# Kernel optimization log

Measured on AMD Instinct MI355X. Metric: run time of the kernel, lower is better.

The kernel has to match this reference:

```python
import jax, jax.numpy as jnp
import numpy as np

B, C, IMG, P = 64, 3, 224, 16
S = P // 2
G = IMG // P                      # 14 patches per side
NP = G * G                        # 196
N = NP + 1                        # +cls token
DIM, DEPTH, H, DH = 384, 12, 12, 32
INNER = H * DH                    # 384
MLP, NCLS = 1536, 1000
PD = 7 * P * P                    # patch_dim = 1792
EPS = 1e-5


def layernorm(x, g, b):
    mu = x.mean(-1, keepdims=True)
    var = ((x - mu) ** 2).mean(-1, keepdims=True)
    return (x - mu) * jax.lax.rsqrt(var + EPS) * g + b


def setup_inputs() -> dict:
    key = jax.random.key(0)
    ks = jax.random.split(key, 24)
    nrm = lambda k, shp, sc: jax.random.normal(k, shp, jnp.float32) * sc
    d = {
        "img": nrm(ks[0], (B, C, IMG, IMG), 1.0),
        "patch_w": nrm(ks[1], (DIM, PD), 0.02),
        "patch_b": jnp.zeros((DIM,), jnp.float32),
        "pos_emb": nrm(ks[2], (1, N, DIM), 0.02),
        "cls_tok": nrm(ks[3], (1, 1, DIM), 0.02),
        "ln1_g": jnp.ones((DEPTH, DIM), jnp.float32),
        "ln1_b": jnp.zeros((DEPTH, DIM), jnp.float32),
        "qkv_w": nrm(ks[4], (DEPTH, 3 * INNER, DIM), 0.02),
        "scale": jax.random.uniform(ks[5], (DEPTH, H), jnp.float32),
        "out_w": nrm(ks[6], (DEPTH, DIM, INNER), 0.02),
        "out_b": jnp.zeros((DEPTH, DIM), jnp.float32),
        "ln2_g": jnp.ones((DEPTH, DIM), jnp.float32),
        "ln2_b": jnp.zeros((DEPTH, DIM), jnp.float32),
        "ff_w1": nrm(ks[7], (DEPTH, MLP, DIM), 0.02),
        "ff_b1": jnp.zeros((DEPTH, MLP), jnp.float32),
        "ff_w2": nrm(ks[8], (DEPTH, DIM, MLP), 0.02),
        "ff_b2": jnp.zeros((DEPTH, DIM), jnp.float32),
        "lnf_g": jnp.ones((DIM,), jnp.float32),
        "lnf_b": jnp.zeros((DIM,), jnp.float32),
        "head_w": nrm(ks[9], (NCLS, DIM), 0.02),
        "head_b": jnp.zeros((NCLS,), jnp.float32),
    }
    return d


def reference(img, patch_w, patch_b, pos_emb, cls_tok, ln1_g, ln1_b, qkv_w,
              scale, out_w, out_b, ln2_g, ln2_b, ff_w1, ff_b1, ff_w2, ff_b2,
              lnf_g, lnf_b, head_w, head_b):
    # --- PatchShifting: pad, channel-mean, 4 shifted crops, concat to 7ch ---
    xp = jnp.pad(img, ((0, 0), (0, 0), (S, S), (S, S)))
    m = xp.mean(axis=1, keepdims=True)                     # [B,1,H+2S,W+2S]
    x_l2 = m[:, :, S:-S, : -2 * S]
    x_r2 = m[:, :, S:-S, 2 * S:]
    x_t2 = m[:, :, : -2 * S, S:-S]
    x_b2 = m[:, :, 2 * S:, S:-S]
    xc = jnp.concatenate([img, x_l2, x_r2, x_t2, x_b2], axis=1)  # [B,7,IMG,IMG]
    # --- patchify: b c (h p1) (w p2) -> b (h w) (p1 p2 c) ---
    patches = xc.reshape(B, 7, G, P, G, P).transpose(0, 2, 4, 3, 5, 1).reshape(B, NP, PD)
    x = patches @ patch_w.T + patch_b                     # [B,NP,DIM]
    x = jnp.concatenate([jnp.broadcast_to(cls_tok, (B, 1, DIM)), x], axis=1)
    x = x + pos_emb
    eye = jnp.eye(N, dtype=bool)
    for i in range(DEPTH):
        h = layernorm(x, ln1_g[i], ln1_b[i])
        qkv = h @ qkv_w[i].T                               # [B,N,3*INNER]
        q, k, v = jnp.split(qkv, 3, axis=-1)
        q = q.reshape(B, N, H, DH).transpose(0, 2, 1, 3)
        k = k.reshape(B, N, H, DH).transpose(0, 2, 1, 3)
        v = v.reshape(B, N, H, DH).transpose(0, 2, 1, 3)
        dots = jnp.einsum("bhid,bhjd->bhij", q, k) * scale[i][None, :, None, None]
        dots = jnp.where(eye, -jnp.inf, dots)              # diagonal self-mask
        attn = jax.nn.softmax(dots, axis=-1)
        o = jnp.einsum("bhij,bhjd->bhid", attn, v)
        o = o.transpose(0, 2, 1, 3).reshape(B, N, INNER)
        x = o @ out_w[i].T + out_b[i] + x
        h2 = layernorm(x, ln2_g[i], ln2_b[i])
        ff = jax.nn.gelu(h2 @ ff_w1[i].T + ff_b1[i], approximate=False)
        x = ff @ ff_w2[i].T + ff_b2[i] + x
    cls = layernorm(x[:, 0], lnf_g, lnf_b)
    return cls @ head_w.T + head_b                         # [B, NCLS]
```

## Files before the change

### kernel.cpp

```cpp
#include <hip/hip_runtime.h>
#include <hip/hip_bf16.h>

#define B_ 64
#define IMG_ 224
#define P_ 16
#define G_ 14
#define NP_ 196
#define N_ 197
#define DIM_ 384
#define DEPTH_ 12
#define H_ 12
#define DH_ 32
#define INNER_ 384
#define MLP_ 1536
#define NCLS_ 1000
#define PD_ 1792
#define EPS_ 1e-5f

typedef __hip_bfloat16 bf16;
using bf16x8 = __attribute__((ext_vector_type(8))) short;
using f32x4  = __attribute__((ext_vector_type(4))) float;

typedef __attribute__((address_space(1))) const void gas_void;
typedef __attribute__((address_space(3))) void las_void;

__device__ __forceinline__ float b2f(bf16 x) { return __bfloat162float(x); }
__device__ __forceinline__ bf16 f2b(float x) { return __float2bfloat16(x); }
__device__ __forceinline__ short f2b_raw(float f) {
    unsigned x = __float_as_uint(f);
    unsigned r = (x + 0x7FFFu + ((x >> 16) & 1u)) >> 16;
    return (short)r;
}
__device__ __forceinline__ void barrier_raw() {
    asm volatile("s_barrier" ::: "memory");
}
__device__ __forceinline__ void waitcnt_vm4() {
    asm volatile("s_waitcnt vmcnt(4)" ::: "memory");
}
__device__ __forceinline__ void waitcnt_vm0() {
    asm volatile("s_waitcnt vmcnt(0)" ::: "memory");
}

__global__ __launch_bounds__(256) void wconv_kernel(const float* __restrict__ src,
                                                    bf16* __restrict__ dst, int n4) {
    int i = blockIdx.x * 256 + threadIdx.x;
    if (i >= n4) return;
    float4 v = ((const float4*)src)[i];
    short4 o;
    o.x = f2b_raw(v.x); o.y = f2b_raw(v.y);
    o.z = f2b_raw(v.z); o.w = f2b_raw(v.w);
    ((short4*)dst)[i] = o;
}

__global__ __launch_bounds__(256) void mean_kernel(const float* __restrict__ img,
                                                   bf16* __restrict__ meanimg) {
    int idx = blockIdx.x * 256 + threadIdx.x;
    if (idx >= B_ * 50176) return;
    int b = idx / 50176;
    int yx = idx - b * 50176;
    const float* p = img + (size_t)b * 3 * 50176 + yx;
    meanimg[idx] = f2b((p[0] + p[50176] + p[100352]) * (1.0f / 3.0f));
}

__global__ __launch_bounds__(256) void patches_kernel(const float* __restrict__ img,
                                                      const bf16* __restrict__ meanimg,
                                                      bf16* __restrict__ patches,
                                                      int bp0, int nbp) {
    int idx = blockIdx.x * 256 + threadIdx.x;
    if (idx >= nbp * 256) return;
    int pix = idx & 255;
    int px = pix & 15, py = pix >> 4;
    int lbp = idx >> 8;
    int bp = bp0 + lbp;
    int p = bp % NP_;
    int b = bp / NP_;
    int gy = p / G_, gx = p - gy * G_;
    int y = gy * P_ + py, x = gx * P_ + px;
    const float* ib = img + (size_t)b * 3 * 50176 + y * 224 + x;
    bf16* out = patches + (size_t)lbp * PD_ + pix * 7;
    out[0] = f2b(ib[0]);
    out[1] = f2b(ib[50176]);
    out[2] = f2b(ib[100352]);
    const bf16* mb = meanimg + (size_t)b * 50176;
    out[3] = (x >= 8)  ? mb[y * 224 + x - 8]   : f2b(0.0f);
    out[4] = (x < 216) ? mb[y * 224 + x + 8]   : f2b(0.0f);
    out[5] = (y >= 8)  ? mb[(y - 8) * 224 + x] : f2b(0.0f);
    out[6] = (y < 216) ? mb[(y + 8) * 224 + x] : f2b(0.0f);
}

__global__ __launch_bounds__(256) void addpos_kernel(const bf16* __restrict__ pe,
                                                     const float* __restrict__ cls_tok,
                                                     const float* __restrict__ pos_emb,
                                                     float* __restrict__ x) {
    int idx = blockIdx.x * 256 + threadIdx.x;
    if (idx >= B_ * N_ * DIM_) return;
    int c = idx % DIM_;
    int r = idx / DIM_;
    int t = r % N_;
    int b = r / N_;
    float v = (t == 0) ? cls_tok[c]
                       : b2f(pe[((size_t)(b * NP_ + t - 1)) * DIM_ + c]);
    x[idx] = v + pos_emb[t * DIM_ + c];
}

__global__ __launch_bounds__(256) void ln_kernel(const float* __restrict__ in,
                                                 long in_stride,
                                                 const float* __restrict__ g,
                                                 const float* __restrict__ bb,
                                                 bf16* __restrict__ out, int rows) {
    int wave = threadIdx.x >> 6;
    int lane = threadIdx.x & 63;
    int row = blockIdx.x * 4 + wave;
    if (row >= rows) return;
    const float* p = in + (size_t)row * in_stride;
    float v[6];
    float s = 0.0f, s2 = 0.0f;
#pragma unroll
    for (int i = 0; i < 6; i++) {
        v[i] = p[lane + 64 * i];
        s += v[i];
        s2 += v[i] * v[i];
    }
#pragma unroll
    for (int m = 32; m >= 1; m >>= 1) {
        s += __shfl_xor(s, m);
        s2 += __shfl_xor(s2, m);
    }
    float mu = s * (1.0f / 384.0f);
    float var = s2 * (1.0f / 384.0f) - mu * mu;
    var = fmaxf(var, 0.0f);
    float inv = rsqrtf(var + EPS_);
    bf16* q = out + (size_t)row * DIM_;
#pragma unroll
    for (int i = 0; i < 6; i++) {
        int c = lane + 64 * i;
        q[c] = f2b((v[i] - mu) * inv * g[c] + bb[c]);
    }
}

__global__ __launch_bounds__(256) void head_kernel(const bf16* __restrict__ cls,
                                                   const float* __restrict__ W,
                                                   const float* __restrict__ bias,
                                                   float* __restrict__ out) {
    int wv = threadIdx.x >> 6, lane = threadIdx.x & 63;
    int col = blockIdx.x * 4 + wv;
    if (col >= NCLS_) return;
    const float* wp = W + (size_t)col * DIM_;
    float wreg[6];
#pragma unroll
    for (int i = 0; i < 6; i++) wreg[i] = wp[i * 64 + lane];
    float hb = bias[col];
    float res = 0.0f;
    for (int r = 0; r < 64; r++) {
        const bf16* ar = cls + r * DIM_;
        float s = 0.0f;
#pragma unroll
        for (int i = 0; i < 6; i++) s += b2f(ar[i * 64 + lane]) * wreg[i];
#pragma unroll
        for (int m = 32; m >= 1; m >>= 1) s += __shfl_xor(s, m);
        if (lane == r) res = s + hb;
    }
    out[(size_t)lane * NCLS_ + col] = res;
}

template <int MODE, typename OutT>
__global__ __launch_bounds__(256) void mgemm3_kernel(const bf16* __restrict__ A,
                                                     const bf16* __restrict__ W,
                                                     const float* __restrict__ bias,
                                                     const float* __restrict__ res,
                                                     OutT* __restrict__ C,
                                                     int M, int N, int K) {
    __shared__ __align__(16) short lds_a[2][128 * 32];
    __shared__ __align__(16) short lds_b[2][128 * 32];
    int tid = threadIdx.x;
    int wv = tid >> 6, lane = tid & 63;
    int ml = lane & 15, quad = lane >> 4;

    unsigned gx = gridDim.x;
    unsigned nwg = gx * gridDim.y;
    unsigned lid = blockIdx.y * gx + blockIdx.x;
    unsigned qc = nwg >> 3, rc = nwg & 7u;
    unsigned xcd = lid & 7u, loc = lid >> 3;
    unsigned nlid = (xcd < rc ? xcd * (qc + 1u)
                              : rc * (qc + 1u) + (xcd - rc) * qc) + loc;
    unsigned bx = nlid % gx, by = nlid / gx;
    int rowBase = by * 128, colBase = bx * 128;

    int srow = wv * 16 + (lane >> 2);
    int kcol = (lane & 3) * 8;
    int ar0 = rowBase + srow;       if (ar0 >= M) ar0 = M - 1;
    int ar1 = rowBase + 64 + srow;  if (ar1 >= M) ar1 = M - 1;
    const bf16* a0 = A + (size_t)ar0 * K + kcol;
    const bf16* a1 = A + (size_t)ar1 * K + kcol;
    const bf16* b0 = W + (size_t)(colBase + srow) * K + kcol;
    const bf16* b1 = W + (size_t)(colBase + 64 + srow) * K + kcol;
    short* laA[2]  = { lds_a[0] + (wv * 16) * 32,      lds_a[1] + (wv * 16) * 32 };
    short* laA2[2] = { lds_a[0] + (64 + wv * 16) * 32, lds_a[1] + (64 + wv * 16) * 32 };
    short* lbB[2]  = { lds_b[0] + (wv * 16) * 32,      lds_b[1] + (wv * 16) * 32 };
    short* lbB2[2] = { lds_b[0] + (64 + wv * 16) * 32, lds_b[1] + (64 + wv * 16) * 32 };

#define ISSUE_TILE(buf, k0)                                                                   \
    do {                                                                                      \
        __builtin_amdgcn_global_load_lds((gas_void*)(a0 + (k0)), (las_void*)laA[buf], 16, 0, 0);  \
        __builtin_amdgcn_global_load_lds((gas_void*)(a1 + (k0)), (las_void*)laA2[buf], 16, 0, 0); \
        __builtin_amdgcn_global_load_lds((gas_void*)(b0 + (k0)), (las_void*)lbB[buf], 16, 0, 0);  \
        __builtin_amdgcn_global_load_lds((gas_void*)(b1 + (k0)), (las_void*)lbB2[buf], 16, 0, 0); \
    } while (0)

    int wr = (wv >> 1) * 64, wc = (wv & 1) * 64;
    f32x4 acc[4][4] = {};
    int NK = K >> 5;

    ISSUE_TILE(0, 0);
    ISSUE_TILE(1, 32);

    for (int k = 0; k < NK; k++) {
        if (k + 1 < NK) waitcnt_vm4();
        else            waitcnt_vm0();
        barrier_raw();
        int cb = k & 1;
        bf16x8 af[4], bfr[4];
#pragma unroll
        for (int rg = 0; rg < 4; rg++)
            af[rg] = *(const bf16x8*)(lds_a[cb] + (wr + rg * 16 + ml) * 32 + quad * 8);
#pragma unroll
        for (int cg = 0; cg < 4; cg++)
            bfr[cg] = *(const bf16x8*)(lds_b[cb] + (wc + cg * 16 + ml) * 32 + quad * 8);
#pragma unroll
        for (int rg = 0; rg < 4; rg++)
#pragma unroll
            for (int cg = 0; cg < 4; cg++)
                acc[rg][cg] = __builtin_amdgcn_mfma_f32_16x16x32_bf16(af[rg], bfr[cg], acc[rg][cg], 0, 0, 0);
        barrier_raw();
        if (k + 2 < NK) ISSUE_TILE(cb, (k + 2) * 32);
    }
#undef ISSUE_TILE

    float bval[4];
#pragma unroll
    for (int cg = 0; cg < 4; cg++)
        bval[cg] = bias ? bias[colBase + wc + cg * 16 + ml] : 0.0f;

#pragma unroll
    for (int rg = 0; rg < 4; rg++) {
#pragma unroll
        for (int reg = 0; reg < 4; reg++) {
            int r = rowBase + wr + rg * 16 + quad * 4 + reg;
            if (r >= M) continue;
            size_t ro = (size_t)r * N;
#pragma unroll
            for (int cg = 0; cg < 4; cg++) {
                int c = colBase + wc + cg * 16 + ml;
                float v = acc[rg][cg][reg] + bval[cg];
                if constexpr (MODE == 1) v += res[ro + c];
                if constexpr (MODE == 2) v = 0.5f * v * (1.0f + erff(v * 0.70710678118f));
                C[ro + c] = (OutT)v;
            }
        }
    }
}

template <int MODE, typename OutT>
__global__ __launch_bounds__(256) void mgemm_kernel(const bf16* __restrict__ A,
                                                    const float* __restrict__ W,
                                                    const float* __restrict__ bias,
                                                    const float* __restrict__ res,
                                                    OutT* __restrict__ C,
                                                    int M, int N, int K) {
    __shared__ __align__(16) short lds_a[128 * 32];
    __shared__ __align__(16) short lds_b[64 * 32];
    int tid = threadIdx.x;
    int rowBase = blockIdx.y * 128;
    int colBase = blockIdx.x * 64;
    int w = tid >> 6, lane = tid & 63;
    int ml = lane & 15, kseg = lane >> 4;

    int ar = tid >> 1;
    int ah = (tid & 1) * 16;
    int agr = rowBase + ar;
    if (agr > M - 1) agr = M - 1;
    const float4* asrc_base = (const float4*)(A + (size_t)agr * K + ah);
    int br = tid >> 2;
    int bs = (tid & 3) * 8;
    const float4* wsrc_base = (const float4*)(W + (size_t)(colBase + br) * K + bs);

    f32x4 acc[2][4] = {};

    for (int k0 = 0; k0 < K; k0 += 32) {
        const float4* asrc = (const float4*)((const bf16*)asrc_base + k0);
        float4 av0 = asrc[0];
        float4 av1 = asrc[1];
        const float4* wsrc = (const float4*)((const float*)wsrc_base + k0);
        float4 w0 = wsrc[0];
        float4 w1 = wsrc[1];
        bf16x8 wb;
        wb[0] = f2b_raw(w0.x); wb[1] = f2b_raw(w0.y);
        wb[2] = f2b_raw(w0.z); wb[3] = f2b_raw(w0.w);
        wb[4] = f2b_raw(w1.x); wb[5] = f2b_raw(w1.y);
        wb[6] = f2b_raw(w1.z); wb[7] = f2b_raw(w1.w);
        __syncthreads();
        *(float4*)(lds_a + ar * 32 + ah) = av0;
        *(float4*)(lds_a + ar * 32 + ah + 8) = av1;
        *(bf16x8*)(lds_b + br * 32 + bs) = wb;
        __syncthreads();
        bf16x8 af0 = *(const bf16x8*)(lds_a + (w * 32 + ml) * 32 + kseg * 8);
        bf16x8 af1 = *(const bf16x8*)(lds_a + (w * 32 + 16 + ml) * 32 + kseg * 8);
#pragma unroll
        for (int ct = 0; ct < 4; ct++) {
            bf16x8 bf_ = *(const bf16x8*)(lds_b + (ct * 16 + ml) * 32 + kseg * 8);
            acc[0][ct] = __builtin_amdgcn_mfma_f32_16x16x32_bf16(af0, bf_, acc[0][ct], 0, 0, 0);
            acc[1][ct] = __builtin_amdgcn_mfma_f32_16x16x32_bf16(af1, bf_, acc[1][ct], 0, 0, 0);
        }
    }

    float bval[4];
#pragma unroll
    for (int ct = 0; ct < 4; ct++)
        bval[ct] = bias ? bias[colBase + ct * 16 + ml] : 0.0f;

#pragma unroll
    for (int rt = 0; rt < 2; rt++) {
#pragma unroll
        for (int reg = 0; reg < 4; reg++) {
            int r = rowBase + w * 32 + rt * 16 + kseg * 4 + reg;
            if (r >= M) continue;
            size_t ro = (size_t)r * N;
#pragma unroll
            for (int ct = 0; ct < 4; ct++) {
                int c = colBase + ct * 16 + ml;
                float v = acc[rt][ct][reg] + bval[ct];
                if constexpr (MODE == 1) v += res[ro + c];
                if constexpr (MODE == 2) v = 0.5f * v * (1.0f + erff(v * 0.70710678118f));
                C[ro + c] = (OutT)v;
            }
        }
    }
}

#define AKR 208
#define VTS 232
#define PSS 232
__global__ __launch_bounds__(256) void attn_mfma_kernel(const bf16* __restrict__ qkv,
                                                        const float* __restrict__ scale,
                                                        bf16* __restrict__ o) {
    __shared__ __align__(16) short Ks[AKR * 32];
    __shared__ __align__(16) short Vt[32 * VTS];
    __shared__ __align__(16) short Ps[4][16 * PSS];
    int b = blockIdx.x, h = blockIdx.y;
    int tid = threadIdx.x;
    int w = tid >> 6, lane = tid & 63;
    int ml = lane & 15, quad = lane >> 4;

    for (int i = tid; i < 32 * VTS / 2; i += 256) ((int*)Vt)[i] = 0;
    for (int e = lane; e < 16 * 16; e += 64) {
        int r = e >> 4, c = e & 15;
        Ps[w][r * PSS + 208 + c] = 0;
    }
    __syncthreads();
    for (int e = tid; e < AKR * 4; e += 256) {
        int row = e >> 2, seg = e & 3;
        float4 v = {0.0f, 0.0f, 0.0f, 0.0f};
        if (row < N_)
            v = *(const float4*)(qkv + (size_t)(b * N_ + row) * (3 * INNER_) + INNER_ + h * DH_ + seg * 8);
        *(float4*)(Ks + row * 32 + seg * 8) = v;
    }
    for (int e = tid; e < N_ * 32; e += 256) {
        int j = e >> 5, d = e & 31;
        Vt[d * VTS + j] = *(const short*)(qkv + (size_t)(b * N_ + j) * (3 * INNER_) + 2 * INNER_ + h * DH_ + d);
    }
    __syncthreads();

    float sc = scale[h];
    for (int qt = w; qt < 13; qt += 4) {
        int q0 = qt * 16;
        int qrow = q0 + ml;
        if (qrow > N_ - 1) qrow = N_ - 1;
        bf16x8 aq = *(const bf16x8*)(qkv + (size_t)(b * N_ + qrow) * (3 * INNER_) + h * DH_ + quad * 8);
        f32x4 accs[13];
#pragma unroll
        for (int kt = 0; kt < 13; kt++) {
            bf16x8 bk = *(const bf16x8*)(Ks + (kt * 16 + ml) * 32 + quad * 8);
            f32x4 z = {0.0f, 0.0f, 0.0f, 0.0f};
            accs[kt] = __builtin_amdgcn_mfma_f32_16x16x32_bf16(aq, bk, z, 0, 0, 0);
        }
        float rmax[4] = {-1e30f, -1e30f, -1e30f, -1e30f};
#pragma unroll
        for (int kt = 0; kt < 13; kt++) {
            int key = kt * 16 + ml;
#pragma unroll
            for (int reg = 0; reg < 4; reg++) {
                int qg = q0 + quad * 4 + reg;
                bool valid = (key < N_) && (key != qg);
                float s = valid ? accs[kt][reg] * sc : -1e30f;
                accs[kt][reg] = s;
                rmax[reg] = fmaxf(rmax[reg], s);
            }
        }
#pragma unroll
        for (int m = 1; m <= 8; m <<= 1)
#pragma unroll
            for (int reg = 0; reg < 4; reg++)
                rmax[reg] = fmaxf(rmax[reg], __shfl_xor(rmax[reg], m));
        float rsum[4] = {0.0f, 0.0f, 0.0f, 0.0f};
#pragma unroll
        for (int kt = 0; kt < 13; kt++) {
#pragma unroll
            for (int reg = 0; reg < 4; reg++) {
                float wgt = __expf(accs[kt][reg] - rmax[reg]);
                accs[kt][reg] = wgt;
                rsum[reg] += wgt;
            }
        }
#pragma unroll
        for (int m = 1; m <= 8; m <<= 1)
#pragma unroll
            for (int reg = 0; reg < 4; reg++)
                rsum[reg] += __shfl_xor(rsum[reg], m);
#pragma unroll
        for (int kt = 0; kt < 13; kt++)
#pragma unroll
            for (int reg = 0; reg < 4; reg++)
                Ps[w][(quad * 4 + reg) * PSS + kt * 16 + ml] = f2b_raw(accs[kt][reg]);
        f32x4 acco[2] = {{0.0f, 0.0f, 0.0f, 0.0f}, {0.0f, 0.0f, 0.0f, 0.0f}};
#pragma unroll
        for (int kc = 0; kc < 7; kc++) {
            bf16x8 ap = *(const bf16x8*)(Ps[w] + ml * PSS + kc * 32 + quad * 8);
#pragma unroll
            for (int nt = 0; nt < 2; nt++) {
                bf16x8 bv = *(const bf16x8*)(Vt + (nt * 16 + ml) * VTS + kc * 32 + quad * 8);
                acco[nt] = __builtin_amdgcn_mfma_f32_16x16x32_bf16(ap, bv, acco[nt], 0, 0, 0);
            }
        }
#pragma unroll
        for (int reg = 0; reg < 4; reg++) {
            int qg = q0 + quad * 4 + reg;
            if (qg >= N_) continue;
            float inv = 1.0f / rsum[reg];
#pragma unroll
            for (int nt = 0; nt < 2; nt++)
                o[(size_t)(b * N_ + qg) * INNER_ + h * DH_ + nt * 16 + ml] = f2b(acco[nt][reg] * inv);
        }
    }
}

__global__ __launch_bounds__(256) void diag_kernel(const float* __restrict__ bufx,
                                                   float* __restrict__ outf,
                                                   int base_marker, int ran) {
    __shared__ int bad;
    if (threadIdx.x == 0) bad = 0;
    __syncthreads();
    if (ran) {
        for (int i = threadIdx.x; i < 4096; i += 256) {
            float v = bufx[i];
            if (!(fabsf(v) < 1e30f)) bad = 1;
        }
    }
    __syncthreads();
    int marker = base_marker + (bad ? 512 : 0);
    if (marker == 0) return;
    int idx = blockIdx.x * 256 + threadIdx.x;
    if (idx > 0 && idx < 64000) outf[idx] = 0.0f;
    if (idx == 0) outf[0] = (float)marker;
}

extern "C" void kernel_launch(void* const* d_in, const int* in_sizes, int n_in,
                              void* d_out, int out_size, void* d_ws, size_t ws_size,
                              hipStream_t stream) {
    const float* img     = (const float*)d_in[0];
    const float* patch_w = (const float*)d_in[1];
    const float* patch_b = (const float*)d_in[2];
    const float* pos_emb = (const float*)d_in[3];
    const float* cls_tok = (const float*)d_in[4];
    const float* ln1_g   = (const float*)d_in[5];
    const float* ln1_b   = (const float*)d_in[6];
    const float* qkv_w   = (const float*)d_in[7];
    const float* scale   = (const float*)d_in[8];
    const float* out_w   = (const float*)d_in[9];
    const float* out_b   = (const float*)d_in[10];
    const float* ln2_g   = (const float*)d_in[11];
    const float* ln2_b   = (const float*)d_in[12];
    const float* ff_w1   = (const float*)d_in[13];
    const float* ff_b1   = (const float*)d_in[14];
    const float* ff_w2   = (const float*)d_in[15];
    const float* ff_b2   = (const float*)d_in[16];
    const float* lnf_g   = (const float*)d_in[17];
    const float* lnf_b   = (const float*)d_in[18];
    const float* head_w  = (const float*)d_in[19];
    const float* head_b  = (const float*)d_in[20];

    const size_t NEED      = 58146816;
    const size_t NEED_FAST = 101990400;
    const size_t NEED_FULL = 140722176;
    char* ws = (char*)d_ws;
    const int ROWS = B_ * N_;
    const int GY = (ROWS + 127) / 128;

    if (ws_size < NEED) {
        diag_kernel<<<250, 256, 0, stream>>>((const float*)d_out, (float*)d_out,
                                             1024 + (int)(ws_size >> 20), 0);
        return;
    }

    float* buf_x  = (float*)ws;
    bf16*  buf_hb = (bf16*)(ws + 19365888);

    if (ws_size >= NEED_FAST) {
        bool full = (ws_size >= NEED_FULL);
        bf16 *buf_qkv, *buf_ff, *buf_patch, *meanimg, *buf_cls;
        bf16 *wb_patch, *wb_qkv, *wb_out, *wb_ff1, *wb_ff2;
        int pchunks, fchunks;
        if (full) {
            buf_qkv  = (bf16*)(ws + 29048832);
            buf_ff   = (bf16*)(ws + 58097664);
            buf_patch= (bf16*)(ws + 29048832);
            meanimg  = (bf16*)(ws + 74006528);
            wb_patch = (bf16*)(ws + 96829440);
            wb_qkv   = (bf16*)(ws + 98205696);
            wb_out   = (bf16*)(ws + 108822528);
            wb_ff1   = (bf16*)(ws + 112361472);
            wb_ff2   = (bf16*)(ws + 126517248);
            buf_cls  = (bf16*)(ws + 140673024);
            pchunks = 1; fchunks = 1;
        } else {
            buf_qkv  = (bf16*)(ws + 29048832);
            buf_ff   = (bf16*)(ws + 29048832);
            buf_patch= (bf16*)(ws + 29048832);
            meanimg  = (bf16*)(ws + 29048832 + 22478848);
            buf_cls  = (bf16*)(ws + 58097664);
            wb_patch = (bf16*)(ws + 58146816);
            wb_qkv   = (bf16*)(ws + 59523072);
            wb_out   = (bf16*)(ws + 70139904);
            wb_ff1   = (bf16*)(ws + 73678848);
            wb_ff2   = (bf16*)(ws + 87834624);
            pchunks = 2; fchunks = 2;
        }

        wconv_kernel<<<(688128 / 4 + 255) / 256, 256, 0, stream>>>(patch_w, wb_patch, 688128 / 4);
        wconv_kernel<<<(5308416 / 4 + 255) / 256, 256, 0, stream>>>(qkv_w, wb_qkv, 5308416 / 4);
        wconv_kernel<<<(1769472 / 4 + 255) / 256, 256, 0, stream>>>(out_w, wb_out, 1769472 / 4);
        wconv_kernel<<<(7077888 / 4 + 255) / 256, 256, 0, stream>>>(ff_w1, wb_ff1, 7077888 / 4);
        wconv_kernel<<<(7077888 / 4 + 255) / 256, 256, 0, stream>>>(ff_w2, wb_ff2, 7077888 / 4);

        mean_kernel<<<(B_ * 50176 + 255) / 256, 256, 0, stream>>>(img, meanimg);
        for (int c = 0; c < pchunks; c++) {
            int bp0 = c * (12544 / pchunks);
            int nbp = 12544 / pchunks;
            patches_kernel<<<nbp, 256, 0, stream>>>(img, meanimg, buf_patch, bp0, nbp);
            mgemm3_kernel<0, bf16><<<dim3(3, (nbp + 127) / 128), 256, 0, stream>>>(
                buf_patch, wb_patch, patch_b, nullptr, buf_hb + (size_t)bp0 * DIM_, nbp, DIM_, PD_);
        }
        addpos_kernel<<<(B_ * N_ * DIM_ + 255) / 256, 256, 0, stream>>>(buf_hb, cls_tok, pos_emb, buf_x);

        for (int i = 0; i < DEPTH_; i++) {
            ln_kernel<<<ROWS / 4, 256, 0, stream>>>(buf_x, DIM_, ln1_g + i * DIM_,
                                                    ln1_b + i * DIM_, buf_hb, ROWS);
            mgemm3_kernel<0, bf16><<<dim3(9, GY), 256, 0, stream>>>(
                buf_hb, wb_qkv + (size_t)i * 3 * INNER_ * DIM_, nullptr, nullptr, buf_qkv,
                ROWS, 3 * INNER_, DIM_);
            attn_mfma_kernel<<<dim3(B_, H_), 256, 0, stream>>>(buf_qkv, scale + i * H_, buf_hb);
            mgemm3_kernel<1, float><<<dim3(3, GY), 256, 0, stream>>>(
                buf_hb, wb_out + (size_t)i * DIM_ * INNER_, out_b + i * DIM_, buf_x, buf_x,
                ROWS, DIM_, INNER_);
            ln_kernel<<<ROWS / 4, 256, 0, stream>>>(buf_x, DIM_, ln2_g + i * DIM_,
                                                    ln2_b + i * DIM_, buf_hb, ROWS);
            int base = 0;
            for (int c = 0; c < fchunks; c++) {
                int mrows = (fchunks == 1) ? ROWS : ((c == 0) ? 6336 : 6272);
                int gy = (mrows + 127) / 128;
                mgemm3_kernel<2, bf16><<<dim3(12, gy), 256, 0, stream>>>(
                    buf_hb + (size_t)base * DIM_, wb_ff1 + (size_t)i * MLP_ * DIM_,
                    ff_b1 + i * MLP_, nullptr, buf_ff, mrows, MLP_, DIM_);
                mgemm3_kernel<1, float><<<dim3(3, gy), 256, 0, stream>>>(
                    buf_ff, wb_ff2 + (size_t)i * DIM_ * MLP_, ff_b2 + i * DIM_,
                    buf_x + (size_t)base * DIM_, buf_x + (size_t)base * DIM_, mrows, DIM_, MLP_);
                base += mrows;
            }
        }

        ln_kernel<<<B_ / 4, 256, 0, stream>>>(buf_x, (long)N_ * DIM_, lnf_g, lnf_b, buf_cls, B_);
        head_kernel<<<250, 256, 0, stream>>>(buf_cls, head_w, head_b, (float*)d_out);
        diag_kernel<<<250, 256, 0, stream>>>(buf_x, (float*)d_out, 0, 1);
        return;
    }

    bf16* buf_cd   = (bf16*)(ws + 29048832);
    bf16* meanimg  = (bf16*)(ws + 29048832 + 22478848);
    bf16* buf_cls  = (bf16*)(ws + 58097664);

    mean_kernel<<<(B_ * 50176 + 255) / 256, 256, 0, stream>>>(img, meanimg);
    for (int c = 0; c < 2; c++) {
        int bp0 = c * 6272;
        patches_kernel<<<6272, 256, 0, stream>>>(img, meanimg, buf_cd, bp0, 6272);
        mgemm_kernel<0, bf16><<<dim3(DIM_ / 64, 49), 256, 0, stream>>>(
            buf_cd, patch_w, patch_b, nullptr, buf_hb + (size_t)bp0 * DIM_, 6272, DIM_, PD_);
    }
    addpos_kernel<<<(B_ * N_ * DIM_ + 255) / 256, 256, 0, stream>>>(buf_hb, cls_tok, pos_emb, buf_x);

    for (int i = 0; i < DEPTH_; i++) {
        ln_kernel<<<ROWS / 4, 256, 0, stream>>>(buf_x, DIM_, ln1_g + i * DIM_,
                                                ln1_b + i * DIM_, buf_hb, ROWS);
        mgemm_kernel<0, bf16><<<dim3((3 * INNER_) / 64, GY), 256, 0, stream>>>(
            buf_hb, qkv_w + (size_t)i * 3 * INNER_ * DIM_, nullptr, nullptr, buf_cd,
            ROWS, 3 * INNER_, DIM_);
        attn_mfma_kernel<<<dim3(B_, H_), 256, 0, stream>>>(buf_cd, scale + i * H_, buf_hb);
        mgemm_kernel<1, float><<<dim3(DIM_ / 64, GY), 256, 0, stream>>>(
            buf_hb, out_w + (size_t)i * DIM_ * INNER_, out_b + i * DIM_, buf_x, buf_x,
            ROWS, DIM_, INNER_);
        ln_kernel<<<ROWS / 4, 256, 0, stream>>>(buf_x, DIM_, ln2_g + i * DIM_,
                                                ln2_b + i * DIM_, buf_hb, ROWS);
        int base = 0;
        for (int c = 0; c < 2; c++) {
            int mrows = (c == 0) ? 6336 : 6272;
            int gy = (mrows + 127) / 128;
            mgemm_kernel<2, bf16><<<dim3(MLP_ / 64, gy), 256, 0, stream>>>(
                buf_hb + (size_t)base * DIM_, ff_w1 + (size_t)i * MLP_ * DIM_,
                ff_b1 + i * MLP_, nullptr, buf_cd, mrows, MLP_, DIM_);
            mgemm_kernel<1, float><<<dim3(DIM_ / 64, gy), 256, 0, stream>>>(
                buf_cd, ff_w2 + (size_t)i * DIM_ * MLP_, ff_b2 + i * DIM_,
                buf_x + (size_t)base * DIM_, buf_x + (size_t)base * DIM_, mrows, DIM_, MLP_);
            base += mrows;
        }
    }

    ln_kernel<<<B_ / 4, 256, 0, stream>>>(buf_x, (long)N_ * DIM_, lnf_g, lnf_b, buf_cls, B_);
    head_kernel<<<250, 256, 0, stream>>>(buf_cls, head_w, head_b, (float*)d_out);
    diag_kernel<<<250, 256, 0, stream>>>(buf_x, (float*)d_out, 0, 1);
}
```

Measured before the change: 2.282 ms.

## Switch GEMMs to 128x64 tiles with triple-buffered LDS and a single barrier

The bf16 MFMA GEMM now uses 128x64 output tiles instead of 128x128, doubling the grid in the column dimension, and cycles through three LDS buffers instead of two. The next tile load is issued right after the barrier, before the current tile's compute, which removes the second barrier per k-step. This aims to raise occupancy and block count on the small-N GEMMs (out-proj and FF2 with N=384) and to overlap loads with MFMA. The cost is lower arithmetic intensity per block (more A re-reads) and fewer MFMAs per LDS read.

```diff
diff --git a/kernel.cpp b/kernel.cpp
--- a/kernel.cpp
+++ b/kernel.cpp
@@ -34,8 +34,8 @@
 __device__ __forceinline__ void barrier_raw() {
     asm volatile("s_barrier" ::: "memory");
 }
-__device__ __forceinline__ void waitcnt_vm4() {
-    asm volatile("s_waitcnt vmcnt(4)" ::: "memory");
+__device__ __forceinline__ void waitcnt_vm3() {
+    asm volatile("s_waitcnt vmcnt(3)" ::: "memory");
 }
 __device__ __forceinline__ void waitcnt_vm0() {
     asm volatile("s_waitcnt vmcnt(0)" ::: "memory");
@@ -164,14 +164,14 @@
 }
 
 template <int MODE, typename OutT>
-__global__ __launch_bounds__(256) void mgemm3_kernel(const bf16* __restrict__ A,
+__global__ __launch_bounds__(256) void mgemm4_kernel(const bf16* __restrict__ A,
                                                      const bf16* __restrict__ W,
                                                      const float* __restrict__ bias,
                                                      const float* __restrict__ res,
                                                      OutT* __restrict__ C,
                                                      int M, int N, int K) {
-    __shared__ __align__(16) short lds_a[2][128 * 32];
-    __shared__ __align__(16) short lds_b[2][128 * 32];
+    __shared__ __align__(16) short lds_a[3][128 * 32];
+    __shared__ __align__(16) short lds_b[3][64 * 32];
     int tid = threadIdx.x;
     int wv = tid >> 6, lane = tid & 63;
     int ml = lane & 15, quad = lane >> 4;
@@ -184,7 +184,7 @@
     unsigned nlid = (xcd < rc ? xcd * (qc + 1u)
                               : rc * (qc + 1u) + (xcd - rc) * qc) + loc;
     unsigned bx = nlid % gx, by = nlid / gx;
-    int rowBase = by * 128, colBase = bx * 128;
+    int rowBase = by * 128, colBase = bx * 64;
 
     int srow = wv * 16 + (lane >> 2);
     int kcol = (lane & 3) * 8;
@@ -193,52 +193,56 @@
     const bf16* a0 = A + (size_t)ar0 * K + kcol;
     const bf16* a1 = A + (size_t)ar1 * K + kcol;
     const bf16* b0 = W + (size_t)(colBase + srow) * K + kcol;
-    const bf16* b1 = W + (size_t)(colBase + 64 + srow) * K + kcol;
-    short* laA[2]  = { lds_a[0] + (wv * 16) * 32,      lds_a[1] + (wv * 16) * 32 };
-    short* laA2[2] = { lds_a[0] + (64 + wv * 16) * 32, lds_a[1] + (64 + wv * 16) * 32 };
-    short* lbB[2]  = { lds_b[0] + (wv * 16) * 32,      lds_b[1] + (wv * 16) * 32 };
-    short* lbB2[2] = { lds_b[0] + (64 + wv * 16) * 32, lds_b[1] + (64 + wv * 16) * 32 };
-
-#define ISSUE_TILE(buf, k0)                                                                   \
-    do {                                                                                      \
-        __builtin_amdgcn_global_load_lds((gas_void*)(a0 + (k0)), (las_void*)laA[buf], 16, 0, 0);  \
-        __builtin_amdgcn_global_load_lds((gas_void*)(a1 + (k0)), (las_void*)laA2[buf], 16, 0, 0); \
-        __builtin_amdgcn_global_load_lds((gas_void*)(b0 + (k0)), (las_void*)lbB[buf], 16, 0, 0);  \
-        __builtin_amdgcn_global_load_lds((gas_void*)(b1 + (k0)), (las_void*)lbB2[buf], 16, 0, 0); \
+    short* lds_a0 = &lds_a[0][0];
+    short* lds_b0 = &lds_b[0][0];
+    int aoff  = (wv * 16) * 32;
+    int aoff2 = (64 + wv * 16) * 32;
+    int boff  = (wv * 16) * 32;
+
+#define ISSUE_TILE(bufi, k0)                                                                            \
+    do {                                                                                                \
+        __builtin_amdgcn_global_load_lds((gas_void*)(a0 + (k0)), (las_void*)(lds_a0 + (bufi) * 4096 + aoff),  16, 0, 0); \
+        __builtin_amdgcn_global_load_lds((gas_void*)(a1 + (k0)), (las_void*)(lds_a0 + (bufi) * 4096 + aoff2), 16, 0, 0); \
+        __builtin_amdgcn_global_load_lds((gas_void*)(b0 + (k0)), (las_void*)(lds_b0 + (bufi) * 2048 + boff),  16, 0, 0); \
     } while (0)
 
-    int wr = (wv >> 1) * 64, wc = (wv & 1) * 64;
-    f32x4 acc[4][4] = {};
+    int wr = (wv >> 1) * 64, wc = (wv & 1) * 32;
+    f32x4 acc[4][2] = {};
     int NK = K >> 5;
 
     ISSUE_TILE(0, 0);
     ISSUE_TILE(1, 32);
 
+    int buf = 0;
     for (int k = 0; k < NK; k++) {
-        if (k + 1 < NK) waitcnt_vm4();
+        if (k + 1 < NK) waitcnt_vm3();
         else            waitcnt_vm0();
         barrier_raw();
-        int cb = k & 1;
-        bf16x8 af[4], bfr[4];
+        if (k + 2 < NK) {
+            int nb = buf + 2; if (nb >= 3) nb -= 3;
+            ISSUE_TILE(nb, (k + 2) * 32);
+        }
+        const short* pa = lds_a0 + buf * 4096;
+        const short* pb = lds_b0 + buf * 2048;
+        bf16x8 af[4], bfr[2];
 #pragma unroll
         for (int rg = 0; rg < 4; rg++)
-            af[rg] = *(const bf16x8*)(lds_a[cb] + (wr + rg * 16 + ml) * 32 + quad * 8);
-#pragma unroll
-        for (int cg = 0; cg < 4; cg++)
-            bfr[cg] = *(const bf16x8*)(lds_b[cb] + (wc + cg * 16 + ml) * 32 + quad * 8);
+            af[rg] = *(const bf16x8*)(pa + (wr + rg * 16 + ml) * 32 + quad * 8);
+#pragma unroll
+        for (int cg = 0; cg < 2; cg++)
+            bfr[cg] = *(const bf16x8*)(pb + (wc + cg * 16 + ml) * 32 + quad * 8);
 #pragma unroll
         for (int rg = 0; rg < 4; rg++)
 #pragma unroll
-            for (int cg = 0; cg < 4; cg++)
+            for (int cg = 0; cg < 2; cg++)
                 acc[rg][cg] = __builtin_amdgcn_mfma_f32_16x16x32_bf16(af[rg], bfr[cg], acc[rg][cg], 0, 0, 0);
-        barrier_raw();
-        if (k + 2 < NK) ISSUE_TILE(cb, (k + 2) * 32);
+        buf++; if (buf == 3) buf = 0;
     }
 #undef ISSUE_TILE
 
-    float bval[4];
-#pragma unroll
-    for (int cg = 0; cg < 4; cg++)
+    float bval[2];
+#pragma unroll
+    for (int cg = 0; cg < 2; cg++)
         bval[cg] = bias ? bias[colBase + wc + cg * 16 + ml] : 0.0f;
 
 #pragma unroll
@@ -249,7 +253,7 @@
             if (r >= M) continue;
             size_t ro = (size_t)r * N;
 #pragma unroll
-            for (int cg = 0; cg < 4; cg++) {
+            for (int cg = 0; cg < 2; cg++) {
                 int c = colBase + wc + cg * 16 + ml;
                 float v = acc[rg][cg][reg] + bval[cg];
                 if constexpr (MODE == 1) v += res[ro + c];
@@ -546,7 +550,7 @@
             int bp0 = c * (12544 / pchunks);
             int nbp = 12544 / pchunks;
             patches_kernel<<<nbp, 256, 0, stream>>>(img, meanimg, buf_patch, bp0, nbp);
-            mgemm3_kernel<0, bf16><<<dim3(3, (nbp + 127) / 128), 256, 0, stream>>>(
+            mgemm4_kernel<0, bf16><<<dim3(6, (nbp + 127) / 128), 256, 0, stream>>>(
                 buf_patch, wb_patch, patch_b, nullptr, buf_hb + (size_t)bp0 * DIM_, nbp, DIM_, PD_);
         }
         addpos_kernel<<<(B_ * N_ * DIM_ + 255) / 256, 256, 0, stream>>>(buf_hb, cls_tok, pos_emb, buf_x);
@@ -554,11 +558,11 @@
         for (int i = 0; i < DEPTH_; i++) {
             ln_kernel<<<ROWS / 4, 256, 0, stream>>>(buf_x, DIM_, ln1_g + i * DIM_,
                                                     ln1_b + i * DIM_, buf_hb, ROWS);
-            mgemm3_kernel<0, bf16><<<dim3(9, GY), 256, 0, stream>>>(
+            mgemm4_kernel<0, bf16><<<dim3(18, GY), 256, 0, stream>>>(
                 buf_hb, wb_qkv + (size_t)i * 3 * INNER_ * DIM_, nullptr, nullptr, buf_qkv,
                 ROWS, 3 * INNER_, DIM_);
             attn_mfma_kernel<<<dim3(B_, H_), 256, 0, stream>>>(buf_qkv, scale + i * H_, buf_hb);
-            mgemm3_kernel<1, float><<<dim3(3, GY), 256, 0, stream>>>(
+            mgemm4_kernel<1, float><<<dim3(6, GY), 256, 0, stream>>>(
                 buf_hb, wb_out + (size_t)i * DIM_ * INNER_, out_b + i * DIM_, buf_x, buf_x,
                 ROWS, DIM_, INNER_);
             ln_kernel<<<ROWS / 4, 256, 0, stream>>>(buf_x, DIM_, ln2_g + i * DIM_,
@@ -567,10 +571,10 @@
             for (int c = 0; c < fchunks; c++) {
                 int mrows = (fchunks == 1) ? ROWS : ((c == 0) ? 6336 : 6272);
                 int gy = (mrows + 127) / 128;
-                mgemm3_kernel<2, bf16><<<dim3(12, gy), 256, 0, stream>>>(
+                mgemm4_kernel<2, bf16><<<dim3(24, gy), 256, 0, stream>>>(
                     buf_hb + (size_t)base * DIM_, wb_ff1 + (size_t)i * MLP_ * DIM_,
                     ff_b1 + i * MLP_, nullptr, buf_ff, mrows, MLP_, DIM_);
-                mgemm3_kernel<1, float><<<dim3(3, gy), 256, 0, stream>>>(
+                mgemm4_kernel<1, float><<<dim3(6, gy), 256, 0, stream>>>(
                     buf_ff, wb_ff2 + (size_t)i * DIM_ * MLP_, ff_b2 + i * DIM_,
                     buf_x + (size_t)base * DIM_, buf_x + (size_t)base * DIM_, mrows, DIM_, MLP_);
                 base += mrows;
```

Result: slower. 2.330 ms (+2.1%).

## Deepen GEMM K-tile to 64 with XOR-swizzled LDS and MFMA priority

Applied to the files above, without the earlier changes.

The bf16 MFMA GEMM now stages 64-wide K tiles instead of 32, doubling the LDS buffers and halving the number of barrier/wait iterations per K loop. Global-to-LDS loads are written with an XOR swizzle on the 16-byte chunk index so fragment reads avoid LDS bank conflicts. The MFMA blocks are wrapped in s_setprio and lgkmcnt fences to separate fragment loads from compute. The cost is twice the LDS per block, which may lower occupancy, and K must be a multiple of 64.

```diff
diff --git a/kernel.cpp b/kernel.cpp
--- a/kernel.cpp
+++ b/kernel.cpp
@@ -34,11 +34,15 @@
 __device__ __forceinline__ void barrier_raw() {
     asm volatile("s_barrier" ::: "memory");
 }
-__device__ __forceinline__ void waitcnt_vm4() {
-    asm volatile("s_waitcnt vmcnt(4)" ::: "memory");
+__device__ __forceinline__ void waitcnt_vm8() {
+    asm volatile("s_waitcnt vmcnt(8)" ::: "memory");
 }
 __device__ __forceinline__ void waitcnt_vm0() {
     asm volatile("s_waitcnt vmcnt(0)" ::: "memory");
+}
+__device__ __forceinline__ void lgkm0_fence() {
+    asm volatile("s_waitcnt lgkmcnt(0)" ::: "memory");
+    __builtin_amdgcn_sched_barrier(0);
 }
 
 __global__ __launch_bounds__(256) void wconv_kernel(const float* __restrict__ src,
@@ -164,14 +168,14 @@
 }
 
 template <int MODE, typename OutT>
-__global__ __launch_bounds__(256) void mgemm3_kernel(const bf16* __restrict__ A,
+__global__ __launch_bounds__(256) void mgemm5_kernel(const bf16* __restrict__ A,
                                                      const bf16* __restrict__ W,
                                                      const float* __restrict__ bias,
                                                      const float* __restrict__ res,
                                                      OutT* __restrict__ C,
                                                      int M, int N, int K) {
-    __shared__ __align__(16) short lds_a[2][128 * 32];
-    __shared__ __align__(16) short lds_b[2][128 * 32];
+    __shared__ __align__(16) short lds_a[2][128 * 64];
+    __shared__ __align__(16) short lds_b[2][128 * 64];
     int tid = threadIdx.x;
     int wv = tid >> 6, lane = tid & 63;
     int ml = lane & 15, quad = lane >> 4;
@@ -186,55 +190,86 @@
     unsigned bx = nlid % gx, by = nlid / gx;
     int rowBase = by * 128, colBase = bx * 128;
 
-    int srow = wv * 16 + (lane >> 2);
-    int kcol = (lane & 3) * 8;
-    int ar0 = rowBase + srow;       if (ar0 >= M) ar0 = M - 1;
-    int ar1 = rowBase + 64 + srow;  if (ar1 >= M) ar1 = M - 1;
-    const bf16* a0 = A + (size_t)ar0 * K + kcol;
-    const bf16* a1 = A + (size_t)ar1 * K + kcol;
-    const bf16* b0 = W + (size_t)(colBase + srow) * K + kcol;
-    const bf16* b1 = W + (size_t)(colBase + 64 + srow) * K + kcol;
-    short* laA[2]  = { lds_a[0] + (wv * 16) * 32,      lds_a[1] + (wv * 16) * 32 };
-    short* laA2[2] = { lds_a[0] + (64 + wv * 16) * 32, lds_a[1] + (64 + wv * 16) * 32 };
-    short* lbB[2]  = { lds_b[0] + (wv * 16) * 32,      lds_b[1] + (wv * 16) * 32 };
-    short* lbB2[2] = { lds_b[0] + (64 + wv * 16) * 32, lds_b[1] + (64 + wv * 16) * 32 };
-
-#define ISSUE_TILE(buf, k0)                                                                   \
-    do {                                                                                      \
-        __builtin_amdgcn_global_load_lds((gas_void*)(a0 + (k0)), (las_void*)laA[buf], 16, 0, 0);  \
-        __builtin_amdgcn_global_load_lds((gas_void*)(a1 + (k0)), (las_void*)laA2[buf], 16, 0, 0); \
-        __builtin_amdgcn_global_load_lds((gas_void*)(b0 + (k0)), (las_void*)lbB[buf], 16, 0, 0);  \
-        __builtin_amdgcn_global_load_lds((gas_void*)(b1 + (k0)), (las_void*)lbB2[buf], 16, 0, 0); \
+    int l8 = lane >> 3;
+    int c8 = lane & 7;
+    int swsrc = ((c8 ^ l8) << 3);
+    const bf16* aS[4];
+    const bf16* bS[4];
+#pragma unroll
+    for (int j = 0; j < 4; j++) {
+        int lr = wv * 32 + j * 8 + l8;
+        int gr = rowBase + lr; if (gr >= M) gr = M - 1;
+        aS[j] = A + (size_t)gr * K + swsrc;
+        bS[j] = W + (size_t)(colBase + lr) * K + swsrc;
+    }
+    short* ldsA0 = &lds_a[0][0];
+    short* ldsB0 = &lds_b[0][0];
+    int dstOff = (wv * 32) * 64;
+
+#define ISSUE_TILE5(bufi, t)                                                                        \
+    do {                                                                                            \
+        _Pragma("unroll")                                                                           \
+        for (int j = 0; j < 4; j++) {                                                               \
+            __builtin_amdgcn_global_load_lds((gas_void*)(aS[j] + (size_t)(t) * 64),                 \
+                (las_void*)(ldsA0 + (bufi) * 8192 + dstOff + j * 512), 16, 0, 0);                   \
+            __builtin_amdgcn_global_load_lds((gas_void*)(bS[j] + (size_t)(t) * 64),                 \
+                (las_void*)(ldsB0 + (bufi) * 8192 + dstOff + j * 512), 16, 0, 0);                   \
+        }                                                                                           \
     } while (0)
 
     int wr = (wv >> 1) * 64, wc = (wv & 1) * 64;
+    int sw0 = ((quad ^ (ml & 7)) << 3);
+    int sw1 = (((4 + quad) ^ (ml & 7)) << 3);
     f32x4 acc[4][4] = {};
-    int NK = K >> 5;
-
-    ISSUE_TILE(0, 0);
-    ISSUE_TILE(1, 32);
-
-    for (int k = 0; k < NK; k++) {
-        if (k + 1 < NK) waitcnt_vm4();
+    int NT = K >> 6;
+
+    ISSUE_TILE5(0, 0);
+    ISSUE_TILE5(1, 1);
+
+    for (int t = 0; t < NT; t++) {
+        if (t + 1 < NT) waitcnt_vm8();
         else            waitcnt_vm0();
         barrier_raw();
-        int cb = k & 1;
-        bf16x8 af[4], bfr[4];
+        int cb = t & 1;
+        const short* pa = &lds_a[cb][0];
+        const short* pb = &lds_b[cb][0];
+
+        bf16x8 af0[4], bf0[4];
 #pragma unroll
         for (int rg = 0; rg < 4; rg++)
-            af[rg] = *(const bf16x8*)(lds_a[cb] + (wr + rg * 16 + ml) * 32 + quad * 8);
+            af0[rg] = *(const bf16x8*)(pa + (wr + rg * 16 + ml) * 64 + sw0);
 #pragma unroll
         for (int cg = 0; cg < 4; cg++)
-            bfr[cg] = *(const bf16x8*)(lds_b[cb] + (wc + cg * 16 + ml) * 32 + quad * 8);
+            bf0[cg] = *(const bf16x8*)(pb + (wc + cg * 16 + ml) * 64 + sw0);
+        lgkm0_fence();
+        __builtin_amdgcn_s_setprio(1);
 #pragma unroll
         for (int rg = 0; rg < 4; rg++)
 #pragma unroll
             for (int cg = 0; cg < 4; cg++)
-                acc[rg][cg] = __builtin_amdgcn_mfma_f32_16x16x32_bf16(af[rg], bfr[cg], acc[rg][cg], 0, 0, 0);
+                acc[rg][cg] = __builtin_amdgcn_mfma_f32_16x16x32_bf16(af0[rg], bf0[cg], acc[rg][cg], 0, 0, 0);
+        __builtin_amdgcn_s_setprio(0);
+
+        bf16x8 af1[4], bf1[4];
+#pragma unroll
+        for (int rg = 0; rg < 4; rg++)
+            af1[rg] = *(const bf16x8*)(pa + (wr + rg * 16 + ml) * 64 + sw1);
+#pragma unroll
+        for (int cg = 0; cg < 4; cg++)
+            bf1[cg] = *(const bf16x8*)(pb + (wc + cg * 16 + ml) * 64 + sw1);
+        lgkm0_fence();
+        __builtin_amdgcn_s_setprio(1);
+#pragma unroll
+        for (int rg = 0; rg < 4; rg++)
+#pragma unroll
+            for (int cg = 0; cg < 4; cg++)
+                acc[rg][cg] = __builtin_amdgcn_mfma_f32_16x16x32_bf16(af1[rg], bf1[cg], acc[rg][cg], 0, 0, 0);
+        __builtin_amdgcn_s_setprio(0);
+
         barrier_raw();
-        if (k + 2 < NK) ISSUE_TILE(cb, (k + 2) * 32);
-    }
-#undef ISSUE_TILE
+        if (t + 2 < NT) ISSUE_TILE5(cb, t + 2);
+    }
+#undef ISSUE_TILE5
 
     float bval[4];
 #pragma unroll
@@ -546,7 +581,7 @@
             int bp0 = c * (12544 / pchunks);
             int nbp = 12544 / pchunks;
             patches_kernel<<<nbp, 256, 0, stream>>>(img, meanimg, buf_patch, bp0, nbp);
-            mgemm3_kernel<0, bf16><<<dim3(3, (nbp + 127) / 128), 256, 0, stream>>>(
+            mgemm5_kernel<0, bf16><<<dim3(3, (nbp + 127) / 128), 256, 0, stream>>>(
                 buf_patch, wb_patch, patch_b, nullptr, buf_hb + (size_t)bp0 * DIM_, nbp, DIM_, PD_);
         }
         addpos_kernel<<<(B_ * N_ * DIM_ + 255) / 256, 256, 0, stream>>>(buf_hb, cls_tok, pos_emb, buf_x);
@@ -554,11 +589,11 @@
         for (int i = 0; i < DEPTH_; i++) {
             ln_kernel<<<ROWS / 4, 256, 0, stream>>>(buf_x, DIM_, ln1_g + i * DIM_,
                                                     ln1_b + i * DIM_, buf_hb, ROWS);
-            mgemm3_kernel<0, bf16><<<dim3(9, GY), 256, 0, stream>>>(
+            mgemm5_kernel<0, bf16><<<dim3(9, GY), 256, 0, stream>>>(
                 buf_hb, wb_qkv + (size_t)i * 3 * INNER_ * DIM_, nullptr, nullptr, buf_qkv,
                 ROWS, 3 * INNER_, DIM_);
             attn_mfma_kernel<<<dim3(B_, H_), 256, 0, stream>>>(buf_qkv, scale + i * H_, buf_hb);
-            mgemm3_kernel<1, float><<<dim3(3, GY), 256, 0, stream>>>(
+            mgemm5_kernel<1, float><<<dim3(3, GY), 256, 0, stream>>>(
                 buf_hb, wb_out + (size_t)i * DIM_ * INNER_, out_b + i * DIM_, buf_x, buf_x,
                 ROWS, DIM_, INNER_);
             ln_kernel<<<ROWS / 4, 256, 0, stream>>>(buf_x, DIM_, ln2_g + i * DIM_,
@@ -567,10 +602,10 @@
             for (int c = 0; c < fchunks; c++) {
                 int mrows = (fchunks == 1) ? ROWS : ((c == 0) ? 6336 : 6272);
                 int gy = (mrows + 127) / 128;
-                mgemm3_kernel<2, bf16><<<dim3(12, gy), 256, 0, stream>>>(
+                mgemm5_kernel<2, bf16><<<dim3(12, gy), 256, 0, stream>>>(
                     buf_hb + (size_t)base * DIM_, wb_ff1 + (size_t)i * MLP_ * DIM_,
                     ff_b1 + i * MLP_, nullptr, buf_ff, mrows, MLP_, DIM_);
-                mgemm3_kernel<1, float><<<dim3(3, gy), 256, 0, stream>>>(
+                mgemm5_kernel<1, float><<<dim3(3, gy), 256, 0, stream>>>(
                     buf_ff, wb_ff2 + (size_t)i * DIM_ * MLP_, ff_b2 + i * DIM_,
                     buf_x + (size_t)base * DIM_, buf_x + (size_t)base * DIM_, mrows, DIM_, MLP_);
                 base += mrows;
```

Result: faster. 2.223 ms (-2.6%).

## Replace LDS-staged GEMM with direct global-to-register double-buffered MFMA loads

Applied to the files above, without the earlier changes.

The GEMM kernel no longer stages A/B tiles in shared memory through async global-to-LDS loads and barriers. Each wave instead loads its 16x32 MFMA fragments directly from global memory into registers, double-buffered across k steps. This removes LDS traffic and block-wide barriers, but tiles shared between waves are now fetched redundantly and the kernel relies on L1/L2 for reuse.

```diff
diff --git a/kernel.cpp b/kernel.cpp
--- a/kernel.cpp
+++ b/kernel.cpp
@@ -21,24 +21,12 @@
 using bf16x8 = __attribute__((ext_vector_type(8))) short;
 using f32x4  = __attribute__((ext_vector_type(4))) float;
 
-typedef __attribute__((address_space(1))) const void gas_void;
-typedef __attribute__((address_space(3))) void las_void;
-
 __device__ __forceinline__ float b2f(bf16 x) { return __bfloat162float(x); }
 __device__ __forceinline__ bf16 f2b(float x) { return __float2bfloat16(x); }
 __device__ __forceinline__ short f2b_raw(float f) {
     unsigned x = __float_as_uint(f);
     unsigned r = (x + 0x7FFFu + ((x >> 16) & 1u)) >> 16;
     return (short)r;
-}
-__device__ __forceinline__ void barrier_raw() {
-    asm volatile("s_barrier" ::: "memory");
-}
-__device__ __forceinline__ void waitcnt_vm4() {
-    asm volatile("s_waitcnt vmcnt(4)" ::: "memory");
-}
-__device__ __forceinline__ void waitcnt_vm0() {
-    asm volatile("s_waitcnt vmcnt(0)" ::: "memory");
 }
 
 __global__ __launch_bounds__(256) void wconv_kernel(const float* __restrict__ src,
@@ -164,14 +152,12 @@
 }
 
 template <int MODE, typename OutT>
-__global__ __launch_bounds__(256) void mgemm3_kernel(const bf16* __restrict__ A,
+__global__ __launch_bounds__(256) void mgemm7_kernel(const bf16* __restrict__ A,
                                                      const bf16* __restrict__ W,
                                                      const float* __restrict__ bias,
                                                      const float* __restrict__ res,
                                                      OutT* __restrict__ C,
                                                      int M, int N, int K) {
-    __shared__ __align__(16) short lds_a[2][128 * 32];
-    __shared__ __align__(16) short lds_b[2][128 * 32];
     int tid = threadIdx.x;
     int wv = tid >> 6, lane = tid & 63;
     int ml = lane & 15, quad = lane >> 4;
@@ -186,55 +172,54 @@
     unsigned bx = nlid % gx, by = nlid / gx;
     int rowBase = by * 128, colBase = bx * 128;
 
-    int srow = wv * 16 + (lane >> 2);
-    int kcol = (lane & 3) * 8;
-    int ar0 = rowBase + srow;       if (ar0 >= M) ar0 = M - 1;
-    int ar1 = rowBase + 64 + srow;  if (ar1 >= M) ar1 = M - 1;
-    const bf16* a0 = A + (size_t)ar0 * K + kcol;
-    const bf16* a1 = A + (size_t)ar1 * K + kcol;
-    const bf16* b0 = W + (size_t)(colBase + srow) * K + kcol;
-    const bf16* b1 = W + (size_t)(colBase + 64 + srow) * K + kcol;
-    short* laA[2]  = { lds_a[0] + (wv * 16) * 32,      lds_a[1] + (wv * 16) * 32 };
-    short* laA2[2] = { lds_a[0] + (64 + wv * 16) * 32, lds_a[1] + (64 + wv * 16) * 32 };
-    short* lbB[2]  = { lds_b[0] + (wv * 16) * 32,      lds_b[1] + (wv * 16) * 32 };
-    short* lbB2[2] = { lds_b[0] + (64 + wv * 16) * 32, lds_b[1] + (64 + wv * 16) * 32 };
-
-#define ISSUE_TILE(buf, k0)                                                                   \
-    do {                                                                                      \
-        __builtin_amdgcn_global_load_lds((gas_void*)(a0 + (k0)), (las_void*)laA[buf], 16, 0, 0);  \
-        __builtin_amdgcn_global_load_lds((gas_void*)(a1 + (k0)), (las_void*)laA2[buf], 16, 0, 0); \
-        __builtin_amdgcn_global_load_lds((gas_void*)(b0 + (k0)), (las_void*)lbB[buf], 16, 0, 0);  \
-        __builtin_amdgcn_global_load_lds((gas_void*)(b1 + (k0)), (las_void*)lbB2[buf], 16, 0, 0); \
-    } while (0)
-
     int wr = (wv >> 1) * 64, wc = (wv & 1) * 64;
+
+    const bf16* ap[4];
+    const bf16* bp[4];
+#pragma unroll
+    for (int rg = 0; rg < 4; rg++) {
+        int r = rowBase + wr + rg * 16 + ml;
+        if (r >= M) r = M - 1;
+        ap[rg] = A + (size_t)r * K + quad * 8;
+    }
+#pragma unroll
+    for (int cg = 0; cg < 4; cg++) {
+        int c = colBase + wc + cg * 16 + ml;
+        bp[cg] = W + (size_t)c * K + quad * 8;
+    }
+
     f32x4 acc[4][4] = {};
     int NK = K >> 5;
 
-    ISSUE_TILE(0, 0);
-    ISSUE_TILE(1, 32);
-
-    for (int k = 0; k < NK; k++) {
-        if (k + 1 < NK) waitcnt_vm4();
-        else            waitcnt_vm0();
-        barrier_raw();
-        int cb = k & 1;
-        bf16x8 af[4], bfr[4];
-#pragma unroll
-        for (int rg = 0; rg < 4; rg++)
-            af[rg] = *(const bf16x8*)(lds_a[cb] + (wr + rg * 16 + ml) * 32 + quad * 8);
-#pragma unroll
-        for (int cg = 0; cg < 4; cg++)
-            bfr[cg] = *(const bf16x8*)(lds_b[cb] + (wc + cg * 16 + ml) * 32 + quad * 8);
-#pragma unroll
-        for (int rg = 0; rg < 4; rg++)
-#pragma unroll
-            for (int cg = 0; cg < 4; cg++)
-                acc[rg][cg] = __builtin_amdgcn_mfma_f32_16x16x32_bf16(af[rg], bfr[cg], acc[rg][cg], 0, 0, 0);
-        barrier_raw();
-        if (k + 2 < NK) ISSUE_TILE(cb, (k + 2) * 32);
-    }
-#undef ISSUE_TILE
+    bf16x8 a0[4], b0[4], a1[4], b1[4];
+
+#define LOADF(as, bs, k0)                                                     \
+    do {                                                                      \
+        _Pragma("unroll")                                                     \
+        for (int rg = 0; rg < 4; rg++) as[rg] = *(const bf16x8*)(ap[rg] + (k0)); \
+        _Pragma("unroll")                                                     \
+        for (int cg = 0; cg < 4; cg++) bs[cg] = *(const bf16x8*)(bp[cg] + (k0)); \
+    } while (0)
+
+#define MFMA16(as, bs)                                                        \
+    do {                                                                      \
+        _Pragma("unroll")                                                     \
+        for (int rg = 0; rg < 4; rg++)                                        \
+            _Pragma("unroll")                                                 \
+            for (int cg = 0; cg < 4; cg++)                                    \
+                acc[rg][cg] = __builtin_amdgcn_mfma_f32_16x16x32_bf16(        \
+                    as[rg], bs[cg], acc[rg][cg], 0, 0, 0);                    \
+    } while (0)
+
+    LOADF(a0, b0, 0);
+    for (int k = 0; k < NK; k += 2) {
+        LOADF(a1, b1, (k + 1) * 32);
+        MFMA16(a0, b0);
+        if (k + 2 < NK) LOADF(a0, b0, (k + 2) * 32);
+        MFMA16(a1, b1);
+    }
+#undef LOADF
+#undef MFMA16
 
     float bval[4];
 #pragma unroll
@@ -424,11 +409,11 @@
         f32x4 acco[2] = {{0.0f, 0.0f, 0.0f, 0.0f}, {0.0f, 0.0f, 0.0f, 0.0f}};
 #pragma unroll
         for (int kc = 0; kc < 7; kc++) {
-            bf16x8 ap = *(const bf16x8*)(Ps[w] + ml * PSS + kc * 32 + quad * 8);
+            bf16x8 ap2 = *(const bf16x8*)(Ps[w] + ml * PSS + kc * 32 + quad * 8);
 #pragma unroll
             for (int nt = 0; nt < 2; nt++) {
                 bf16x8 bv = *(const bf16x8*)(Vt + (nt * 16 + ml) * VTS + kc * 32 + quad * 8);
-                acco[nt] = __builtin_amdgcn_mfma_f32_16x16x32_bf16(ap, bv, acco[nt], 0, 0, 0);
+                acco[nt] = __builtin_amdgcn_mfma_f32_16x16x32_bf16(ap2, bv, acco[nt], 0, 0, 0);
             }
         }
 #pragma unroll
@@ -546,7 +531,7 @@
             int bp0 = c * (12544 / pchunks);
             int nbp = 12544 / pchunks;
             patches_kernel<<<nbp, 256, 0, stream>>>(img, meanimg, buf_patch, bp0, nbp);
-            mgemm3_kernel<0, bf16><<<dim3(3, (nbp + 127) / 128), 256, 0, stream>>>(
+            mgemm7_kernel<0, bf16><<<dim3(3, (nbp + 127) / 128), 256, 0, stream>>>(
                 buf_patch, wb_patch, patch_b, nullptr, buf_hb + (size_t)bp0 * DIM_, nbp, DIM_, PD_);
         }
         addpos_kernel<<<(B_ * N_ * DIM_ + 255) / 256, 256, 0, stream>>>(buf_hb, cls_tok, pos_emb, buf_x);
@@ -554,11 +539,11 @@
         for (int i = 0; i < DEPTH_; i++) {
             ln_kernel<<<ROWS / 4, 256, 0, stream>>>(buf_x, DIM_, ln1_g + i * DIM_,
                                                     ln1_b + i * DIM_, buf_hb, ROWS);
-            mgemm3_kernel<0, bf16><<<dim3(9, GY), 256, 0, stream>>>(
+            mgemm7_kernel<0, bf16><<<dim3(9, GY), 256, 0, stream>>>(
                 buf_hb, wb_qkv + (size_t)i * 3 * INNER_ * DIM_, nullptr, nullptr, buf_qkv,
                 ROWS, 3 * INNER_, DIM_);
             attn_mfma_kernel<<<dim3(B_, H_), 256, 0, stream>>>(buf_qkv, scale + i * H_, buf_hb);
-            mgemm3_kernel<1, float><<<dim3(3, GY), 256, 0, stream>>>(
+            mgemm7_kernel<1, float><<<dim3(3, GY), 256, 0, stream>>>(
                 buf_hb, wb_out + (size_t)i * DIM_ * INNER_, out_b + i * DIM_, buf_x, buf_x,
                 ROWS, DIM_, INNER_);
             ln_kernel<<<ROWS / 4, 256, 0, stream>>>(buf_x, DIM_, ln2_g + i * DIM_,
@@ -567,10 +552,10 @@
             for (int c = 0; c < fchunks; c++) {
                 int mrows = (fchunks == 1) ? ROWS : ((c == 0) ? 6336 : 6272);
                 int gy = (mrows + 127) / 128;
-                mgemm3_kernel<2, bf16><<<dim3(12, gy), 256, 0, stream>>>(
+                mgemm7_kernel<2, bf16><<<dim3(12, gy), 256, 0, stream>>>(
                     buf_hb + (size_t)base * DIM_, wb_ff1 + (size_t)i * MLP_ * DIM_,
                     ff_b1 + i * MLP_, nullptr, buf_ff, mrows, MLP_, DIM_);
-                mgemm3_kernel<1, float><<<dim3(3, gy), 256, 0, stream>>>(
+                mgemm7_kernel<1, float><<<dim3(3, gy), 256, 0, stream>>>(
                     buf_ff, wb_ff2 + (size_t)i * DIM_ * MLP_, ff_b2 + i * DIM_,
                     buf_x + (size_t)base * DIM_, buf_x + (size_t)base * DIM_, mrows, DIM_, MLP_);
                 base += mrows;
```

After: 3.843 ms. 68.4% more time.
